# Kernel tuning notes

Measured on AMD Instinct MI355X. Metric: run time of the kernel, lower is better.

## Reference

```python
import jax, jax.numpy as jnp
import numpy as np

B, N, E, H = 2, 256, 256, 768


def setup_inputs() -> dict:
    key = jax.random.key(0)
    ks = jax.random.split(key, 9)
    s_e = 1.0 / np.sqrt(E)
    s_h = 1.0 / np.sqrt(H)
    return {
        "x": jax.random.normal(ks[0], (B, N, E), dtype=jnp.float32),
        "Wq": jax.random.uniform(ks[1], (E, H), jnp.float32, -s_e, s_e),
        "bq": jax.random.uniform(ks[2], (H,), jnp.float32, -s_e, s_e),
        "Wk": jax.random.uniform(ks[3], (E, H), jnp.float32, -s_e, s_e),
        "bk": jax.random.uniform(ks[4], (H,), jnp.float32, -s_e, s_e),
        "Wv": jax.random.uniform(ks[5], (E, H), jnp.float32, -s_e, s_e),
        "bv": jax.random.uniform(ks[6], (H,), jnp.float32, -s_e, s_e),
        "we": jax.random.uniform(ks[7], (H,), jnp.float32, -s_h, s_h),
        "be": jax.random.uniform(ks[8], (), jnp.float32, -s_h, s_h),
    }


def reference(x, Wq, bq, Wk, bk, Wv, bv, we, be):
    # Projections: [B,N,H]
    q = x @ Wq + bq
    k = x @ Wk + bk
    v = x @ Wv + bv
    # Per (i,j): q_i + k_j + v_j  (key and value both broadcast over query axis)
    kv = k + v  # [B,N,H]
    # energy: [B,N,N] = leaky_relu(q_i + kv_j) . we + be
    energy = jnp.einsum(
        "bijh,h->bij",
        jax.nn.leaky_relu(q[:, :, None, :] + kv[:, None, :, :], negative_slope=0.01),
        we,
    ) + be
    attn = jax.nn.softmax(energy, axis=-1)  # softmax over keys j
    return jnp.einsum("bij,bjh->bih", attn, v)  # [B,N,H]
```

## Files before the change

### kernel.cpp

```cpp
#include <hip/hip_runtime.h>

#define B 2
#define N 256
#define E 256
#define H 768
#define H4 (H / 4)

#define PROJ_STEP(ee, wv, A)                                                  \
    { const float4 xA = *(const float4*)&xs[ee][0];                           \
      const float4 xB = *(const float4*)&xs[ee][4];                           \
      A[0].x = fmaf(xA.x, wv.x, A[0].x); A[0].y = fmaf(xA.x, wv.y, A[0].y);   \
      A[0].z = fmaf(xA.x, wv.z, A[0].z); A[0].w = fmaf(xA.x, wv.w, A[0].w);   \
      A[1].x = fmaf(xA.y, wv.x, A[1].x); A[1].y = fmaf(xA.y, wv.y, A[1].y);   \
      A[1].z = fmaf(xA.y, wv.z, A[1].z); A[1].w = fmaf(xA.y, wv.w, A[1].w);   \
      A[2].x = fmaf(xA.z, wv.x, A[2].x); A[2].y = fmaf(xA.z, wv.y, A[2].y);   \
      A[2].z = fmaf(xA.z, wv.z, A[2].z); A[2].w = fmaf(xA.z, wv.w, A[2].w);   \
      A[3].x = fmaf(xA.w, wv.x, A[3].x); A[3].y = fmaf(xA.w, wv.y, A[3].y);   \
      A[3].z = fmaf(xA.w, wv.z, A[3].z); A[3].w = fmaf(xA.w, wv.w, A[3].w);   \
      A[4].x = fmaf(xB.x, wv.x, A[4].x); A[4].y = fmaf(xB.x, wv.y, A[4].y);   \
      A[4].z = fmaf(xB.x, wv.z, A[4].z); A[4].w = fmaf(xB.x, wv.w, A[4].w);   \
      A[5].x = fmaf(xB.y, wv.x, A[5].x); A[5].y = fmaf(xB.y, wv.y, A[5].y);   \
      A[5].z = fmaf(xB.y, wv.z, A[5].z); A[5].w = fmaf(xB.y, wv.w, A[5].w);   \
      A[6].x = fmaf(xB.z, wv.x, A[6].x); A[6].y = fmaf(xB.z, wv.y, A[6].y);   \
      A[6].z = fmaf(xB.z, wv.z, A[6].z); A[6].w = fmaf(xB.z, wv.w, A[6].w);   \
      A[7].x = fmaf(xB.w, wv.x, A[7].x); A[7].y = fmaf(xB.w, wv.y, A[7].y);   \
      A[7].z = fmaf(xB.w, wv.z, A[7].z); A[7].w = fmaf(xB.w, wv.w, A[7].w); }

__global__ __launch_bounds__(256) void proj_kernel(
    const float* __restrict__ x,
    const float* __restrict__ Wq, const float* __restrict__ bq,
    const float* __restrict__ Wk, const float* __restrict__ bk,
    const float* __restrict__ Wv, const float* __restrict__ bv,
    const float* __restrict__ we, float* __restrict__ wb,
    float* __restrict__ q, float* __restrict__ v, float4* __restrict__ kvT)
{
    __shared__ float  xs[E][8];
    __shared__ float4 red[8][4][64];

    const int t    = threadIdx.x;
    const int lane = t & 63;
    const int rg   = t >> 6;
    const int type = (blockIdx.x < 192) ? 1 : 0;
    const int bid  = blockIdx.x % 192;
    const int ct   = bid >> 6;
    const int rt   = bid & 63;
    const int r0   = rt * 8;
    const int c    = ct * 256 + lane * 4;

    if (blockIdx.x == 0 && t < H4) {
        float4 w = ((const float4*)we)[t];
        w.x *= 0.495f; w.y *= 0.495f; w.z *= 0.495f; w.w *= 0.495f;
        ((float4*)wb)[t] = w;
    }

    {
        float4 lo, hi;
        lo.x = x[(r0 + 0) * E + t]; lo.y = x[(r0 + 1) * E + t];
        lo.z = x[(r0 + 2) * E + t]; lo.w = x[(r0 + 3) * E + t];
        hi.x = x[(r0 + 4) * E + t]; hi.y = x[(r0 + 5) * E + t];
        hi.z = x[(r0 + 6) * E + t]; hi.w = x[(r0 + 7) * E + t];
        *(float4*)&xs[t][0] = lo;
        *(float4*)&xs[t][4] = hi;
    }
    __syncthreads();

    const int e0 = rg * 64;

    if (type == 0) {
        float4 A[8] = {};
        const float4* Wp = (const float4*)(Wq + c);
        float4 w0 = Wp[(e0 + 0) * H4], w1 = Wp[(e0 + 1) * H4];
        float4 w2 = Wp[(e0 + 2) * H4], w3 = Wp[(e0 + 3) * H4];
        int e = e0;
        #pragma unroll 1
        for (; e < e0 + 60; e += 4) {
            float4 n0 = Wp[(e + 4) * H4], n1 = Wp[(e + 5) * H4];
            float4 n2 = Wp[(e + 6) * H4], n3 = Wp[(e + 7) * H4];
            PROJ_STEP(e    , w0, A);
            PROJ_STEP(e + 1, w1, A);
            PROJ_STEP(e + 2, w2, A);
            PROJ_STEP(e + 3, w3, A);
            w0 = n0; w1 = n1; w2 = n2; w3 = n3;
        }
        PROJ_STEP(e    , w0, A);
        PROJ_STEP(e + 1, w1, A);
        PROJ_STEP(e + 2, w2, A);
        PROJ_STEP(e + 3, w3, A);

        #pragma unroll
        for (int r = 0; r < 8; ++r) red[r][rg][lane] = A[r];
        __syncthreads();
        const float4 bias = *(const float4*)(bq + c);
        #pragma unroll
        for (int ri = 0; ri < 2; ++ri) {
            const int r = 2 * rg + ri;
            const float4 p0 = red[r][0][lane], p1 = red[r][1][lane];
            const float4 p2 = red[r][2][lane], p3 = red[r][3][lane];
            float4 s;
            s.x = ((p0.x + p1.x) + (p2.x + p3.x)) + bias.x;
            s.y = ((p0.y + p1.y) + (p2.y + p3.y)) + bias.y;
            s.z = ((p0.z + p1.z) + (p2.z + p3.z)) + bias.z;
            s.w = ((p0.w + p1.w) + (p2.w + p3.w)) + bias.w;
            *(float4*)(q + (size_t)(r0 + r) * H + c) = s;
        }
    } else {
        float4 AK[8] = {}, AV[8] = {};
        const float4* Kp = (const float4*)(Wk + c);
        const float4* Vp = (const float4*)(Wv + c);
        float4 k0 = Kp[(e0 + 0) * H4], k1 = Kp[(e0 + 1) * H4];
        float4 u0 = Vp[(e0 + 0) * H4], u1 = Vp[(e0 + 1) * H4];
        int e = e0;
        #pragma unroll 1
        for (; e < e0 + 62; e += 2) {
            float4 nk0 = Kp[(e + 2) * H4], nk1 = Kp[(e + 3) * H4];
            float4 nu0 = Vp[(e + 2) * H4], nu1 = Vp[(e + 3) * H4];
            PROJ_STEP(e    , k0, AK);
            PROJ_STEP(e    , u0, AV);
            PROJ_STEP(e + 1, k1, AK);
            PROJ_STEP(e + 1, u1, AV);
            k0 = nk0; k1 = nk1; u0 = nu0; u1 = nu1;
        }
        PROJ_STEP(e    , k0, AK);
        PROJ_STEP(e    , u0, AV);
        PROJ_STEP(e + 1, k1, AK);
        PROJ_STEP(e + 1, u1, AV);

        #pragma unroll
        for (int r = 0; r < 8; ++r) red[r][rg][lane] = AV[r];
        __syncthreads();
        const float4 bv4 = *(const float4*)(bv + c);
        const float4 bk4 = *(const float4*)(bk + c);
        float4 vs[2];
        #pragma unroll
        for (int ri = 0; ri < 2; ++ri) {
            const int r = 2 * rg + ri;
            const float4 p0 = red[r][0][lane], p1 = red[r][1][lane];
            const float4 p2 = red[r][2][lane], p3 = red[r][3][lane];
            float4 s;
            s.x = ((p0.x + p1.x) + (p2.x + p3.x)) + bv4.x;
            s.y = ((p0.y + p1.y) + (p2.y + p3.y)) + bv4.y;
            s.z = ((p0.z + p1.z) + (p2.z + p3.z)) + bv4.z;
            s.w = ((p0.w + p1.w) + (p2.w + p3.w)) + bv4.w;
            vs[ri] = s;
            *(float4*)(v + (size_t)(r0 + r) * H + c) = s;
        }
        __syncthreads();

        #pragma unroll
        for (int r = 0; r < 8; ++r) red[r][rg][lane] = AK[r];
        __syncthreads();
        #pragma unroll
        for (int ri = 0; ri < 2; ++ri) {
            const int r = 2 * rg + ri;
            const float4 p0 = red[r][0][lane], p1 = red[r][1][lane];
            const float4 p2 = red[r][2][lane], p3 = red[r][3][lane];
            float4 s;
            s.x = ((p0.x + p1.x) + (p2.x + p3.x)) + bk4.x + vs[ri].x;
            s.y = ((p0.y + p1.y) + (p2.y + p3.y)) + bk4.y + vs[ri].y;
            s.z = ((p0.z + p1.z) + (p2.z + p3.z)) + bk4.z + vs[ri].z;
            s.w = ((p0.w + p1.w) + (p2.w + p3.w)) + bk4.w + vs[ri].w;
            const int row = r0 + r;
            const int bb = row >> 8, n = row & 255;
            kvT[((size_t)bb * H4 + (c >> 2)) * N + n] = s;
        }
    }
}
#undef PROJ_STEP

__global__ __launch_bounds__(512) void energy_kernel(
    const float* __restrict__ q, const float4* __restrict__ kvT,
    const float* __restrict__ wb, float* __restrict__ eout)
{
    __shared__ float qs[8][H];
    __shared__ float wbs[H];
    __shared__ float pE[8][16][64];

    const int t    = threadIdx.x;
    const int jl   = t & 31;
    const int hq   = t >> 5;
    const int row0 = (blockIdx.x >> 2) * 8;
    const int j0   = (blockIdx.x & 3) * 64;
    const int b    = row0 >> 8;

    {
        float4* qs4 = (float4*)qs;
        const float4* qg = (const float4*)(q + (size_t)row0 * H);
        #pragma unroll
        for (int i = 0; i < 3; ++i) qs4[t + 512 * i] = qg[t + 512 * i];
        if (t < H4) ((float4*)wbs)[t] = ((const float4*)wb)[t];
    }
    __syncthreads();

    const float4* kv0 = kvT + (size_t)b * H4 * N + (j0 + jl);
    const int base = hq * 12;

    float acc0[8] = {0,0,0,0,0,0,0,0};
    float acc1[8] = {0,0,0,0,0,0,0,0};
    float4 ka0 = {0,0,0,0}, ka1 = {0,0,0,0};

#define ESTEP2(idx, u0_, u1_)                                                   \
    { const float4 wb4 = *(const float4*)&wbs[(idx) * 4];                       \
      ka0.x = fmaf(u0_.x, wb4.x, ka0.x); ka0.y = fmaf(u0_.y, wb4.y, ka0.y);     \
      ka0.z = fmaf(u0_.z, wb4.z, ka0.z); ka0.w = fmaf(u0_.w, wb4.w, ka0.w);     \
      ka1.x = fmaf(u1_.x, wb4.x, ka1.x); ka1.y = fmaf(u1_.y, wb4.y, ka1.y);     \
      ka1.z = fmaf(u1_.z, wb4.z, ka1.z); ka1.w = fmaf(u1_.w, wb4.w, ka1.w);     \
      _Pragma("unroll")                                                         \
      for (int r = 0; r < 8; ++r) {                                             \
          const float4 qa = *(const float4*)&qs[r][(idx) * 4];                  \
          float s;                                                              \
          s = qa.x + u0_.x; acc0[r] = fmaf(__builtin_fabsf(s), wb4.x, acc0[r]); \
          s = qa.x + u1_.x; acc1[r] = fmaf(__builtin_fabsf(s), wb4.x, acc1[r]); \
          s = qa.y + u0_.y; acc0[r] = fmaf(__builtin_fabsf(s), wb4.y, acc0[r]); \
          s = qa.y + u1_.y; acc1[r] = fmaf(__builtin_fabsf(s), wb4.y, acc1[r]); \
          s = qa.z + u0_.z; acc0[r] = fmaf(__builtin_fabsf(s), wb4.z, acc0[r]); \
          s = qa.z + u1_.z; acc1[r] = fmaf(__builtin_fabsf(s), wb4.z, acc1[r]); \
          s = qa.w + u0_.w; acc0[r] = fmaf(__builtin_fabsf(s), wb4.w, acc0[r]); \
          s = qa.w + u1_.w; acc1[r] = fmaf(__builtin_fabsf(s), wb4.w, acc1[r]); \
      } }

    float4 a0 = kv0[(base + 0) * N],      a1 = kv0[(base + 1) * N];
    float4 c0 = kv0[(base + 0) * N + 32], c1 = kv0[(base + 1) * N + 32];
    int it = 0;
    #pragma unroll 1
    for (; it < 10; it += 2) {
        float4 na0 = kv0[(base + it + 2) * N],      na1 = kv0[(base + it + 3) * N];
        float4 nc0 = kv0[(base + it + 2) * N + 32], nc1 = kv0[(base + it + 3) * N + 32];
        ESTEP2(base + it    , a0, c0);
        ESTEP2(base + it + 1, a1, c1);
        a0 = na0; a1 = na1; c0 = nc0; c1 = nc1;
    }
    ESTEP2(base + 10, a0, c0);
    ESTEP2(base + 11, a1, c1);
#undef ESTEP2

    const float KS = 0.505f / 0.495f;
    const float k0s = KS * ((ka0.x + ka0.y) + (ka0.z + ka0.w));
    const float k1s = KS * ((ka1.x + ka1.y) + (ka1.z + ka1.w));
    #pragma unroll
    for (int r = 0; r < 8; ++r) {
        pE[r][hq][jl]      = acc0[r] + k0s;
        pE[r][hq][jl + 32] = acc1[r] + k1s;
    }
    __syncthreads();

    const int rr = t >> 6, jc = t & 63;
    float ev = 0.f;
    #pragma unroll
    for (int k = 0; k < 16; ++k) ev += pE[rr][k][jc];
    eout[(size_t)(row0 + rr) * N + j0 + jc] = ev;
}

#define PSTEP(aj, vv, Am) \
    Am.x = fmaf(aj, vv.x, Am.x); Am.y = fmaf(aj, vv.y, Am.y); \
    Am.z = fmaf(aj, vv.z, Am.z); Am.w = fmaf(aj, vv.w, Am.w);

__global__ __launch_bounds__(256) void pv_kernel(
    const float* __restrict__ eout, const float* __restrict__ v,
    float* __restrict__ out)
{
    __shared__ float es[16][256];
    __shared__ float inv_s[16];

    const int t   = threadIdx.x;
    const int b   = blockIdx.x / 192;
    const int r_  = blockIdx.x % 192;
    const int it_ = r_ / 12;
    const int ht  = r_ % 12;
    const int i0  = it_ * 16;
    const int h4l = t & 15;
    const int il  = t >> 4;

    {
        float4* es4 = (float4*)es;
        const float4* ep = (const float4*)(eout + (size_t)(b * 256 + i0) * N);
        #pragma unroll
        for (int k = 0; k < 4; ++k) es4[t + 256 * k] = ep[t + 256 * k];
    }
    __syncthreads();

    const int wv = t >> 6, ln = t & 63;
    #pragma unroll
    for (int rr = 0; rr < 4; ++rr) {
        const int row = wv * 4 + rr;
        const float4 evv = ((const float4*)es[row])[ln];
        float m = fmaxf(fmaxf(evv.x, evv.y), fmaxf(evv.z, evv.w));
        #pragma unroll
        for (int off = 1; off < 64; off <<= 1) m = fmaxf(m, __shfl_xor(m, off));
        float4 p;
        p.x = __expf(evv.x - m); p.y = __expf(evv.y - m);
        p.z = __expf(evv.z - m); p.w = __expf(evv.w - m);
        float s = (p.x + p.y) + (p.z + p.w);
        #pragma unroll
        for (int off = 1; off < 64; off <<= 1) s += __shfl_xor(s, off);
        ((float4*)es[row])[ln] = p;
        if (ln == 0) inv_s[row] = 1.0f / s;
    }
    __syncthreads();

    const float4* vp = (const float4*)(v + (size_t)(b * 256) * H + ht * 64) + h4l;
    const float4* a4 = (const float4*)es[il];

    float4 P = {0.f, 0.f, 0.f, 0.f}, Q = P;
    float4 av = a4[0];
    float4 v0 = vp[0], v1 = vp[H4], v2 = vp[2 * H4], v3 = vp[3 * H4];
    int j4 = 0;
    #pragma unroll 1
    for (; j4 < 63; ++j4) {
        const float4 nav = a4[j4 + 1];
        const int jb = 4 * j4 + 4;
        float4 n0 = vp[(jb + 0) * H4], n1 = vp[(jb + 1) * H4];
        float4 n2 = vp[(jb + 2) * H4], n3 = vp[(jb + 3) * H4];
        PSTEP(av.x, v0, P); PSTEP(av.y, v1, Q);
        PSTEP(av.z, v2, P); PSTEP(av.w, v3, Q);
        av = nav;
        v0 = n0; v1 = n1; v2 = n2; v3 = n3;
    }
    PSTEP(av.x, v0, P); PSTEP(av.y, v1, Q);
    PSTEP(av.z, v2, P); PSTEP(av.w, v3, Q);

    const float is = inv_s[il];
    float4 R;
    R.x = (P.x + Q.x) * is; R.y = (P.y + Q.y) * is;
    R.z = (P.z + Q.z) * is; R.w = (P.w + Q.w) * is;
    *(float4*)(out + (size_t)(b * 256 + i0 + il) * H + ht * 64 + h4l * 4) = R;
}

extern "C" void kernel_launch(void* const* d_in, const int* in_sizes, int n_in,
                              void* d_out, int out_size, void* d_ws, size_t ws_size,
                              hipStream_t stream) {
    const float* x  = (const float*)d_in[0];
    const float* Wq = (const float*)d_in[1];
    const float* bq = (const float*)d_in[2];
    const float* Wk = (const float*)d_in[3];
    const float* bk = (const float*)d_in[4];
    const float* Wv = (const float*)d_in[5];
    const float* bv = (const float*)d_in[6];
    const float* we = (const float*)d_in[7];
    float* out = (float*)d_out;

    float*  q    = (float*)d_ws;
    float*  v    = q + B * N * H;
    float4* kvT  = (float4*)(v + B * N * H);
    float*  eout = (float*)(kvT + B * H4 * N);
    float*  wb   = eout + B * N * N;

    proj_kernel<<<384, 256, 0, stream>>>(x, Wq, bq, Wk, bk, Wv, bv, we, wb, q, v, kvT);
    energy_kernel<<<256, 512, 0, stream>>>(q, kvT, wb, eout);
    pv_kernel<<<384, 256, 0, stream>>>(eout, v, out);
}
```

Before: 55.42 us.

## Split projection K-dim across 8 slices and retile PV kernel for fewer blocks

The projection kernel now gives each block 128 output columns instead of 256 and splits the 256-long reduction into 8 slices of 32, reduced through shared memory. This doubles the grid to 768 blocks and shortens each thread's serial FMA chain. The PV kernel moves to 256 blocks of 384 threads, each covering 96 columns, so every 16-row softmax is computed fewer times across the grid. The cost is a larger shared reduction stage and some idle waves during the softmax phase.

Result: no change. 55.08 us (-0.6%).

```diff
diff --git a/kernel.cpp b/kernel.cpp
--- a/kernel.cpp
+++ b/kernel.cpp
@@ -35,17 +35,18 @@
     float* __restrict__ q, float* __restrict__ v, float4* __restrict__ kvT)
 {
     __shared__ float  xs[E][8];
-    __shared__ float4 red[8][4][64];
-
-    const int t    = threadIdx.x;
-    const int lane = t & 63;
-    const int rg   = t >> 6;
-    const int type = (blockIdx.x < 192) ? 1 : 0;
-    const int bid  = blockIdx.x % 192;
-    const int ct   = bid >> 6;
-    const int rt   = bid & 63;
-    const int r0   = rt * 8;
-    const int c    = ct * 256 + lane * 4;
+    __shared__ float4 red[8][8][32];
+
+    const int t     = threadIdx.x;
+    const int lane  = t & 63;
+    const int cl    = t & 31;
+    const int ks    = ((t >> 6) << 1) | (lane >> 5);
+    const int heavy = (blockIdx.x < 384);
+    const int bid   = heavy ? blockIdx.x : (blockIdx.x - 384);
+    const int ct    = bid >> 6;
+    const int rt    = bid & 63;
+    const int r0    = rt * 8;
+    const int c     = ct * 128 + cl * 4;
 
     if (blockIdx.x == 0 && t < H4) {
         float4 w = ((const float4*)we)[t];
@@ -64,16 +65,17 @@
     }
     __syncthreads();
 
-    const int e0 = rg * 64;
-
-    if (type == 0) {
+    const int e0 = ks * 32;
+    const int orow = t >> 5;
+
+    if (!heavy) {
         float4 A[8] = {};
         const float4* Wp = (const float4*)(Wq + c);
         float4 w0 = Wp[(e0 + 0) * H4], w1 = Wp[(e0 + 1) * H4];
         float4 w2 = Wp[(e0 + 2) * H4], w3 = Wp[(e0 + 3) * H4];
         int e = e0;
         #pragma unroll 1
-        for (; e < e0 + 60; e += 4) {
+        for (; e < e0 + 28; e += 4) {
             float4 n0 = Wp[(e + 4) * H4], n1 = Wp[(e + 5) * H4];
             float4 n2 = Wp[(e + 6) * H4], n3 = Wp[(e + 7) * H4];
             PROJ_STEP(e    , w0, A);
@@ -88,21 +90,16 @@
         PROJ_STEP(e + 3, w3, A);
 
         #pragma unroll
-        for (int r = 0; r < 8; ++r) red[r][rg][lane] = A[r];
+        for (int r = 0; r < 8; ++r) red[r][ks][cl] = A[r];
         __syncthreads();
         const float4 bias = *(const float4*)(bq + c);
-        #pragma unroll
-        for (int ri = 0; ri < 2; ++ri) {
-            const int r = 2 * rg + ri;
-            const float4 p0 = red[r][0][lane], p1 = red[r][1][lane];
-            const float4 p2 = red[r][2][lane], p3 = red[r][3][lane];
-            float4 s;
-            s.x = ((p0.x + p1.x) + (p2.x + p3.x)) + bias.x;
-            s.y = ((p0.y + p1.y) + (p2.y + p3.y)) + bias.y;
-            s.z = ((p0.z + p1.z) + (p2.z + p3.z)) + bias.z;
-            s.w = ((p0.w + p1.w) + (p2.w + p3.w)) + bias.w;
-            *(float4*)(q + (size_t)(r0 + r) * H + c) = s;
-        }
+        float4 s = bias;
+        #pragma unroll
+        for (int k = 0; k < 8; ++k) {
+            const float4 p = red[orow][k][cl];
+            s.x += p.x; s.y += p.y; s.z += p.z; s.w += p.w;
+        }
+        *(float4*)(q + (size_t)(r0 + orow) * H + c) = s;
     } else {
         float4 AK[8] = {}, AV[8] = {};
         const float4* Kp = (const float4*)(Wk + c);
@@ -111,7 +108,7 @@
         float4 u0 = Vp[(e0 + 0) * H4], u1 = Vp[(e0 + 1) * H4];
         int e = e0;
         #pragma unroll 1
-        for (; e < e0 + 62; e += 2) {
+        for (; e < e0 + 30; e += 2) {
             float4 nk0 = Kp[(e + 2) * H4], nk1 = Kp[(e + 3) * H4];
             float4 nu0 = Vp[(e + 2) * H4], nu1 = Vp[(e + 3) * H4];
             PROJ_STEP(e    , k0, AK);
@@ -126,43 +123,33 @@
         PROJ_STEP(e + 1, u1, AV);
 
         #pragma unroll
-        for (int r = 0; r < 8; ++r) red[r][rg][lane] = AV[r];
+        for (int r = 0; r < 8; ++r) red[r][ks][cl] = AV[r];
         __syncthreads();
         const float4 bv4 = *(const float4*)(bv + c);
         const float4 bk4 = *(const float4*)(bk + c);
-        float4 vs[2];
-        #pragma unroll
-        for (int ri = 0; ri < 2; ++ri) {
-            const int r = 2 * rg + ri;
-            const float4 p0 = red[r][0][lane], p1 = red[r][1][lane];
-            const float4 p2 = red[r][2][lane], p3 = red[r][3][lane];
-            float4 s;
-            s.x = ((p0.x + p1.x) + (p2.x + p3.x)) + bv4.x;
-            s.y = ((p0.y + p1.y) + (p2.y + p3.y)) + bv4.y;
-            s.z = ((p0.z + p1.z) + (p2.z + p3.z)) + bv4.z;
-            s.w = ((p0.w + p1.w) + (p2.w + p3.w)) + bv4.w;
-            vs[ri] = s;
-            *(float4*)(v + (size_t)(r0 + r) * H + c) = s;
-        }
+        float4 vs = bv4;
+        #pragma unroll
+        for (int k = 0; k < 8; ++k) {
+            const float4 p = red[orow][k][cl];
+            vs.x += p.x; vs.y += p.y; vs.z += p.z; vs.w += p.w;
+        }
+        *(float4*)(v + (size_t)(r0 + orow) * H + c) = vs;
         __syncthreads();
 
         #pragma unroll
-        for (int r = 0; r < 8; ++r) red[r][rg][lane] = AK[r];
+        for (int r = 0; r < 8; ++r) red[r][ks][cl] = AK[r];
         __syncthreads();
-        #pragma unroll
-        for (int ri = 0; ri < 2; ++ri) {
-            const int r = 2 * rg + ri;
-            const float4 p0 = red[r][0][lane], p1 = red[r][1][lane];
-            const float4 p2 = red[r][2][lane], p3 = red[r][3][lane];
-            float4 s;
-            s.x = ((p0.x + p1.x) + (p2.x + p3.x)) + bk4.x + vs[ri].x;
-            s.y = ((p0.y + p1.y) + (p2.y + p3.y)) + bk4.y + vs[ri].y;
-            s.z = ((p0.z + p1.z) + (p2.z + p3.z)) + bk4.z + vs[ri].z;
-            s.w = ((p0.w + p1.w) + (p2.w + p3.w)) + bk4.w + vs[ri].w;
-            const int row = r0 + r;
-            const int bb = row >> 8, n = row & 255;
-            kvT[((size_t)bb * H4 + (c >> 2)) * N + n] = s;
-        }
+        float4 s;
+        s.x = bk4.x + vs.x; s.y = bk4.y + vs.y;
+        s.z = bk4.z + vs.z; s.w = bk4.w + vs.w;
+        #pragma unroll
+        for (int k = 0; k < 8; ++k) {
+            const float4 p = red[orow][k][cl];
+            s.x += p.x; s.y += p.y; s.z += p.z; s.w += p.w;
+        }
+        const int row = r0 + orow;
+        const int bb = row >> 8, n = row & 255;
+        kvT[((size_t)bb * H4 + (c >> 2)) * N + n] = s;
     }
 }
 #undef PROJ_STEP
@@ -254,50 +241,51 @@
     Am.x = fmaf(aj, vv.x, Am.x); Am.y = fmaf(aj, vv.y, Am.y); \
     Am.z = fmaf(aj, vv.z, Am.z); Am.w = fmaf(aj, vv.w, Am.w);
 
-__global__ __launch_bounds__(256) void pv_kernel(
+__global__ __launch_bounds__(384) void pv_kernel(
     const float* __restrict__ eout, const float* __restrict__ v,
     float* __restrict__ out)
 {
     __shared__ float es[16][256];
     __shared__ float inv_s[16];
 
-    const int t   = threadIdx.x;
-    const int b   = blockIdx.x / 192;
-    const int r_  = blockIdx.x % 192;
-    const int it_ = r_ / 12;
-    const int ht  = r_ % 12;
-    const int i0  = it_ * 16;
-    const int h4l = t & 15;
-    const int il  = t >> 4;
+    const int t    = threadIdx.x;
+    const int i0g  = (blockIdx.x >> 3) * 16;
+    const int b    = i0g >> 8;
+    const int ht   = blockIdx.x & 7;
+    const int h4l  = t % 24;
+    const int il   = t / 24;
 
     {
         float4* es4 = (float4*)es;
-        const float4* ep = (const float4*)(eout + (size_t)(b * 256 + i0) * N);
-        #pragma unroll
-        for (int k = 0; k < 4; ++k) es4[t + 256 * k] = ep[t + 256 * k];
+        const float4* ep = (const float4*)(eout + (size_t)i0g * N);
+        es4[t]       = ep[t];
+        es4[t + 384] = ep[t + 384];
+        if (t < 256) es4[t + 768] = ep[t + 768];
     }
     __syncthreads();
 
     const int wv = t >> 6, ln = t & 63;
-    #pragma unroll
-    for (int rr = 0; rr < 4; ++rr) {
-        const int row = wv * 4 + rr;
-        const float4 evv = ((const float4*)es[row])[ln];
-        float m = fmaxf(fmaxf(evv.x, evv.y), fmaxf(evv.z, evv.w));
-        #pragma unroll
-        for (int off = 1; off < 64; off <<= 1) m = fmaxf(m, __shfl_xor(m, off));
-        float4 p;
-        p.x = __expf(evv.x - m); p.y = __expf(evv.y - m);
-        p.z = __expf(evv.z - m); p.w = __expf(evv.w - m);
-        float s = (p.x + p.y) + (p.z + p.w);
-        #pragma unroll
-        for (int off = 1; off < 64; off <<= 1) s += __shfl_xor(s, off);
-        ((float4*)es[row])[ln] = p;
-        if (ln == 0) inv_s[row] = 1.0f / s;
-    }
-    __syncthreads();
-
-    const float4* vp = (const float4*)(v + (size_t)(b * 256) * H + ht * 64) + h4l;
+    if (wv < 4) {
+        #pragma unroll
+        for (int rr = 0; rr < 4; ++rr) {
+            const int row = wv * 4 + rr;
+            const float4 evv = ((const float4*)es[row])[ln];
+            float m = fmaxf(fmaxf(evv.x, evv.y), fmaxf(evv.z, evv.w));
+            #pragma unroll
+            for (int off = 1; off < 64; off <<= 1) m = fmaxf(m, __shfl_xor(m, off));
+            float4 p;
+            p.x = __expf(evv.x - m); p.y = __expf(evv.y - m);
+            p.z = __expf(evv.z - m); p.w = __expf(evv.w - m);
+            float s = (p.x + p.y) + (p.z + p.w);
+            #pragma unroll
+            for (int off = 1; off < 64; off <<= 1) s += __shfl_xor(s, off);
+            ((float4*)es[row])[ln] = p;
+            if (ln == 0) inv_s[row] = 1.0f / s;
+        }
+    }
+    __syncthreads();
+
+    const float4* vp = (const float4*)(v + (size_t)(b * 256) * H) + ht * 24 + h4l;
     const float4* a4 = (const float4*)es[il];
 
     float4 P = {0.f, 0.f, 0.f, 0.f}, Q = P;
@@ -322,7 +310,7 @@
     float4 R;
     R.x = (P.x + Q.x) * is; R.y = (P.y + Q.y) * is;
     R.z = (P.z + Q.z) * is; R.w = (P.w + Q.w) * is;
-    *(float4*)(out + (size_t)(b * 256 + i0 + il) * H + ht * 64 + h4l * 4) = R;
+    *(float4*)(out + (size_t)(i0g + il) * H + ht * 96 + h4l * 4) = R;
 }
 
 extern "C" void kernel_launch(void* const* d_in, const int* in_sizes, int n_in,
@@ -344,7 +332,7 @@
     float*  eout = (float*)(kvT + B * H4 * N);
     float*  wb   = eout + B * N * N;
 
-    proj_kernel<<<384, 256, 0, stream>>>(x, Wq, bq, Wk, bk, Wv, bv, we, wb, q, v, kvT);
+    proj_kernel<<<768, 256, 0, stream>>>(x, Wq, bq, Wk, bk, Wv, bv, we, wb, q, v, kvT);
     energy_kernel<<<256, 512, 0, stream>>>(q, kvT, wb, eout);
-    pv_kernel<<<384, 256, 0, stream>>>(eout, v, out);
+    pv_kernel<<<256, 384, 0, stream>>>(eout, v, out);
 }
```
